# Kernel optimization log

Hardware: AMD Instinct MI355X
Metric: run time of the kernel (lower is better)

## Reference

```python
import jax, jax.numpy as jnp
import numpy as np

N, E, H, D, HC = 6000, 12000, 4, 32, 128


def _ln(x, g, b, eps=1e-5):
    m = jnp.mean(x, axis=-1, keepdims=True)
    v = jnp.mean((x - m) ** 2, axis=-1, keepdims=True)
    return (x - m) / jnp.sqrt(v + eps) * g + b


def _gelu(x):
    return jax.nn.gelu(x, approximate=False)


def _gatv2(x, src, dst, ea, wl, bl, wr, br, we, att, bias):
    # x: [N,HC], ea: [E,HC] (already encoded). heads H, per-head dim D.
    xl = (x @ wl + bl).reshape(N, H, D)   # source transform
    xr = (x @ wr + br).reshape(N, H, D)   # target transform
    xe = (ea @ we).reshape(E, H, D)
    g = jax.nn.leaky_relu(xl[src] + xr[dst] + xe, 0.1)   # [E,H,D]
    logits = jnp.einsum('ehd,hd->eh', g, att)            # [E,H]
    m = jax.ops.segment_max(logits, dst, num_segments=N)
    m = jnp.where(jnp.isfinite(m), m, 0.0)
    ex = jnp.exp(logits - m[dst])
    s = jax.ops.segment_sum(ex, dst, num_segments=N)
    alpha = ex / (s[dst] + 1e-16)                        # softmax over in-edges of dst
    out = jax.ops.segment_sum(alpha[..., None] * xl[src], dst, num_segments=N)
    return out.reshape(N, H * D) + bias


def _nnconv(h, src, dst, ea, w, b, root, bias):
    # dynamic per-edge weight matrix: [E, HC, HC]
    W = (ea @ w + b).reshape(E, HC, HC)
    msg = jnp.einsum('ei,eio->eo', h[src], W)            # per-edge matvec
    agg = jax.ops.segment_sum(msg, dst, num_segments=N)  # sum aggregation
    return agg + h @ root + bias


def setup_inputs() -> dict:
    key = jax.random.key(0)
    ks = jax.random.split(key, 16)
    rn = lambda k, shp, s: jax.random.normal(k, shp, jnp.float32) * s
    inv = lambda f: 1.0 / np.sqrt(f).astype(np.float32)
    return {
        'x': rn(ks[0], (N, 6), 1.0),
        'edge_index': jax.random.randint(ks[1], (2, E), 0, N, dtype=jnp.int32),
        'edge_attr': rn(ks[2], (E, 4), 1.0),
        'batch': jnp.zeros((N,), jnp.int32),
        'node_enc_w': rn(ks[3], (6, HC), inv(6)),
        'edge_enc_w': rn(ks[4], (4, HC), inv(4)),
        'edge_enc_b': jnp.zeros((HC,), jnp.float32),
        'gat_lin_l_w': rn(ks[5], (2, HC, HC), inv(HC)),
        'gat_lin_l_b': jnp.zeros((2, HC), jnp.float32),
        'gat_lin_r_w': rn(ks[6], (2, HC, HC), inv(HC)),
        'gat_lin_r_b': jnp.zeros((2, HC), jnp.float32),
        'gat_lin_e_w': rn(ks[7], (2, HC, HC), inv(HC)),
        'gat_att': rn(ks[8], (2, H, D), inv(D)),
        'gat_bias': jnp.zeros((2, HC), jnp.float32),
        'gat_ln_g': jnp.ones((2, HC), jnp.float32),
        'gat_ln_b': jnp.zeros((2, HC), jnp.float32),
        'nn_w': rn(ks[9], (8, HC, HC * HC), inv(HC)),
        'nn_b': jnp.zeros((8, HC * HC), jnp.float32),
        'nn_root': rn(ks[10], (8, HC, HC), inv(HC)),
        'nn_bias': jnp.zeros((8, HC), jnp.float32),
        'dec_ln_g': jnp.ones((8, HC), jnp.float32),
        'dec_ln_b': jnp.zeros((8, HC), jnp.float32),
        'out_w': rn(ks[11], (HC, 2), inv(HC)),
        'out_b': jnp.zeros((2,), jnp.float32),
    }


def reference(x, edge_index, edge_attr, batch, node_enc_w, edge_enc_w, edge_enc_b,
              gat_lin_l_w, gat_lin_l_b, gat_lin_r_w, gat_lin_r_b, gat_lin_e_w,
              gat_att, gat_bias, gat_ln_g, gat_ln_b,
              nn_w, nn_b, nn_root, nn_bias, dec_ln_g, dec_ln_b, out_w, out_b):
    src, dst = edge_index[0], edge_index[1]
    h0 = x @ node_enc_w                              # node encoder (no bias)
    ea = edge_attr @ edge_enc_w + edge_enc_b         # edge encoder
    # GraphTransEncoder layers (dropout in eval mode = identity)
    for i in range(2):
        x1 = _gatv2(h0, src, dst, ea, gat_lin_l_w[i], gat_lin_l_b[i],
                    gat_lin_r_w[i], gat_lin_r_b[i], gat_lin_e_w[i],
                    gat_att[i], gat_bias[i])
        h0 = _gelu(_ln(h0 + x1, gat_ln_g[i], gat_ln_b[i]))
    # initial conv with decoder[0]'s NNConv
    h = _nnconv(h0, src, dst, ea, nn_w[0], nn_b[0], nn_root[0], nn_bias[0])
    # DeepGCN 'res+' layers, each fed x + h
    for i in range(8):
        hin = h0 + h
        t = _gelu(_ln(hin, dec_ln_g[i], dec_ln_b[i]))
        t = _nnconv(t, src, dst, ea, nn_w[i], nn_b[i], nn_root[i], nn_bias[i])
        h = hin + t
    out = _gelu(_ln(h, dec_ln_g[0], dec_ln_b[0]))
    return out @ out_w + out_b
```

## Files before the change

### kernel.cpp

```cpp
#include <hip/hip_runtime.h>
#include <math.h>

#define NN 6000
#define NE 12000
#define DCAP 32

typedef _Float16 f16;
typedef _Float16 f16x8 __attribute__((ext_vector_type(8)));
typedef unsigned short u16x8 __attribute__((ext_vector_type(8)));
typedef float f32x4 __attribute__((ext_vector_type(4)));

__device__ __forceinline__ float gelu_f(float x) {
    return 0.5f * x * (1.0f + erff(x * 0.70710678118654752f));
}

__global__ __launch_bounds__(256) void k_pre_all(
    const float* __restrict__ nn_w, const float* __restrict__ nn_b,
    const float* __restrict__ nn_root, f16* __restrict__ bfh,
    const float* __restrict__ x, const float* __restrict__ node_w,
    float* __restrict__ h0, f16* __restrict__ hf,
    const int* __restrict__ ei, const float* __restrict__ eattr,
    int* __restrict__ cnt, float* __restrict__ ebs,
    const float* __restrict__ gat_e_w, const float* __restrict__ eew,
    const float* __restrict__ eeb, const float* __restrict__ lb,
    const float* __restrict__ rb, float* __restrict__ EW, float* __restrict__ biasLR,
    const float* __restrict__ gwl, const float* __restrict__ gwr,
    f16* __restrict__ WTh)
{
    __shared__ float enc[5][128];
    int b = blockIdx.x;
    int tid = threadIdx.x;
    if (b < 512) {
        for (int l = tid; l < 640; l += 256) {
            int j = l >> 7, k = l & 127;
            enc[j][k] = (j < 4) ? eew[j * 128 + k] : eeb[k];
        }
        __syncthreads();
        int gid = b * 256 + tid;
        int i = gid >> 14;
        int col = gid & 16383;
        int k_in = col >> 7, o = col & 127;
        const float* w = nn_w + (size_t)i * (128 * 16384) + col;
        float a0 = 0.f, a1 = 0.f, a2 = 0.f, a3 = 0.f, a4 = 0.f;
        #pragma unroll 8
        for (int k = 0; k < 128; ++k) {
            float wv = w[(size_t)k * 16384];
            a0 += enc[0][k] * wv; a1 += enc[1][k] * wv; a2 += enc[2][k] * wv;
            a3 += enc[3][k] * wv; a4 += enc[4][k] * wv;
        }
        a4 += nn_b[i * 16384 + col];
        float root = nn_root[(size_t)i * 16384 + col];
        float vals[6] = {a0, a1, a2, a3, a4, root};
        int ot = o >> 4, l15o = o & 15;
        size_t base_i = ((size_t)i * 8 + ot) * 24;
        #pragma unroll
        for (int j = 0; j < 6; ++j) {
            int c = j * 128 + k_in;
            int kb = c >> 5, lg = (c >> 3) & 3, jj = c & 7;
            size_t dst = ((base_i + kb) * 64 + lg * 16 + l15o) * 8 + jj;
            bfh[dst] = (f16)vals[j];
        }
    } else if (b < 3512) {
        int idx = (b - 512) * 256 + tid;
        int n = idx >> 7, c = idx & 127;
        float s = 0.f;
        #pragma unroll
        for (int f = 0; f < 6; ++f) s += x[n * 6 + f] * node_w[f * 128 + c];
        h0[idx] = s;
        hf[idx] = (f16)s;
    } else if (b < 3559) {
        int e = (b - 3512) * 256 + tid;
        if (e < NE) {
            int d = ei[NE + e];
            int pos = atomicAdd(&cnt[d], 1);
            if (pos < DCAP) {
                float* p = ebs + (size_t)(d * DCAP + pos) * 8;
                p[0] = __int_as_float(ei[e]);
                p[1] = eattr[e * 4 + 0];
                p[2] = eattr[e * 4 + 1];
                p[3] = eattr[e * 4 + 2];
                p[4] = eattr[e * 4 + 3];
            }
        }
    } else if (b < 3566) {
        int idx = (b - 3559) * 256 + tid;
        if (idx < 1280) {
            int i = idx / 640; int r = idx % 640; int j = r >> 7; int o = r & 127;
            float s = 0.f;
            for (int k = 0; k < 128; ++k) {
                float e = (j < 4) ? eew[j * 128 + k] : eeb[k];
                s += e * gat_e_w[i * 16384 + k * 128 + o];
            }
            EW[idx] = s;
        } else if (idx < 1792) {
            int j = idx - 1280; int i = j >> 8; int c = j & 255;
            biasLR[j] = (c < 128) ? lb[i * 128 + c] : rb[i * 128 + c - 128];
        }
    } else {
        int bb = b - 3566;
        int i = bb >> 2, half = (bb >> 1) & 1, piece = bb & 1;
        const float* s = (half ? gwr : gwl) + (size_t)i * 16384;
        size_t dbase = (size_t)i * 32768 + (size_t)half * 16384;
        for (int l = tid + piece * 8192; l < 8192 + piece * 8192; l += 256) {
            int o = l >> 7, k = l & 127;
            WTh[dbase + o * 128 + k] = (f16)s[k * 128 + o];
        }
    }
}

__global__ __launch_bounds__(256) void k_mm16(
    const f16* __restrict__ A, const f16* __restrict__ Bh,
    const float* __restrict__ bias, f16* __restrict__ C, int M, int P)
{
    __shared__ __align__(16) unsigned short smem[16384];
    unsigned short* sA  = smem;
    unsigned short* sBh = smem + 8192;
    const int tid = threadIdx.x;
    const int r0 = blockIdx.x * 64, n0 = blockIdx.y * 64;
    #pragma unroll
    for (int i = 0; i < 4; ++i) {
        int g = tid + i * 256; int row = g >> 4, u = g & 15;
        int dst = row * 128 + ((u ^ (row & 7)) << 3);
        int r = r0 + row;
        if (r < M) *(u16x8*)&sA[dst] = *(const u16x8*)((const unsigned short*)A + (size_t)r * 128 + u * 8);
        else { u16x8 z; for (int j = 0; j < 8; ++j) z[j] = 0; *(u16x8*)&sA[dst] = z; }
        size_t sb = (size_t)(n0 + row) * 128 + u * 8;
        *(u16x8*)&sBh[dst] = *(const u16x8*)((const unsigned short*)Bh + sb);
    }
    __syncthreads();
    const int lane = tid & 63, wid = tid >> 6;
    const int wm = wid & 1, wn = wid >> 1;
    const int l15 = lane & 15, lg = lane >> 4;
    f32x4 acc[2][2] = {};
    #pragma unroll
    for (int kk = 0; kk < 4; ++kk) {
        f16x8 a[2], bh_[2];
        #pragma unroll
        for (int fm = 0; fm < 2; ++fm) {
            int row = wm * 32 + fm * 16 + l15;
            int off = row * 128 + ((((kk << 2) + lg) ^ (row & 7)) << 3);
            a[fm] = *(const f16x8*)&sA[off];
        }
        #pragma unroll
        for (int fn = 0; fn < 2; ++fn) {
            int row = wn * 32 + fn * 16 + l15;
            int off = row * 128 + ((((kk << 2) + lg) ^ (row & 7)) << 3);
            bh_[fn] = *(const f16x8*)&sBh[off];
        }
        #pragma unroll
        for (int fm = 0; fm < 2; ++fm)
        #pragma unroll
        for (int fn = 0; fn < 2; ++fn)
            acc[fm][fn] = __builtin_amdgcn_mfma_f32_16x16x32_f16(a[fm], bh_[fn], acc[fm][fn], 0, 0, 0);
    }
    #pragma unroll
    for (int fn = 0; fn < 2; ++fn) {
        int col = n0 + wn * 32 + fn * 16 + l15;
        float bv = bias ? bias[col] : 0.f;
        #pragma unroll
        for (int fm = 0; fm < 2; ++fm) {
            int rbase = r0 + wm * 32 + fm * 16 + lg * 4;
            #pragma unroll
            for (int j = 0; j < 4; ++j) {
                int r = rbase + j;
                if (r < M) C[(size_t)r * P + col] = (f16)(acc[fm][fn][j] + bv);
            }
        }
    }
}

__global__ __launch_bounds__(256) void k_gat_fused(
    const f16* __restrict__ XLXR, const float* __restrict__ ebs,
    const int* __restrict__ cnt, const float* __restrict__ EW,
    const float* __restrict__ att, float* __restrict__ h0,
    const float* __restrict__ bias, const float* __restrict__ g,
    const float* __restrict__ b,
    f16* __restrict__ hf)
{
    __shared__ float slog[4][DCAP][4];
    __shared__ float sms[4][4][2];
    int rowl = threadIdx.x >> 6, lane = threadIdx.x & 63;
    int r = blockIdx.x * 4 + rowl;
    int deg = cnt[r]; if (deg > DCAP) deg = DCAP;
    int dc = (deg < 4) ? deg : 4;
    float hz0 = h0[r * 128 + lane], hz1 = h0[r * 128 + 64 + lane];
    float xr0 = (float)XLXR[r * 256 + 128 + lane];
    float xr1 = (float)XLXR[r * 256 + 192 + lane];
    float e0 = EW[lane], e1 = EW[128 + lane], e2 = EW[256 + lane], e3 = EW[384 + lane], e4 = EW[512 + lane];
    float f0 = EW[64 + lane], f1 = EW[192 + lane], f2 = EW[320 + lane], f3 = EW[448 + lane], f4 = EW[576 + lane];
    float at0 = att[lane], at1 = att[64 + lane];
    f32x4 q[4]; float a3v[4]; float xs0[4], xs1[4];
    #pragma unroll
    for (int j = 0; j < 4; ++j) {
        if (j < dc) {
            const float* ep = ebs + (size_t)(r * DCAP + j) * 8;
            q[j] = *(const f32x4*)ep;
            a3v[j] = ep[4];
        }
    }
    #pragma unroll
    for (int j = 0; j < 4; ++j) {
        if (j < dc) {
            int s = __float_as_int(q[j][0]);
            xs0[j] = (float)XLXR[s * 256 + lane];
            xs1[j] = (float)XLXR[s * 256 + 64 + lane];
        }
    }
    #pragma unroll
    for (int j = 0; j < 4; ++j) {
        if (j < dc) {
            float a0 = q[j][1], a1 = q[j][2], a2 = q[j][3], a3 = a3v[j];
            float g0 = xs0[j] + xr0 + (a0 * e0 + a1 * e1 + a2 * e2 + a3 * e3 + e4);
            float g1 = xs1[j] + xr1 + (a0 * f0 + a1 * f1 + a2 * f2 + a3 * f3 + f4);
            g0 = (g0 > 0.f) ? g0 : 0.1f * g0;
            g1 = (g1 > 0.f) ? g1 : 0.1f * g1;
            float p0 = g0 * at0, p1 = g1 * at1;
            for (int o = 16; o; o >>= 1) { p0 += __shfl_xor(p0, o, 32); p1 += __shfl_xor(p1, o, 32); }
            if ((lane & 31) == 0) {
                int hh2 = lane >> 5;
                slog[rowl][j][hh2] = p0;
                slog[rowl][j][2 + hh2] = p1;
            }
        }
    }
    for (int k = 4; k < deg; ++k) {
        const float* ep = ebs + (size_t)(r * DCAP + k) * 8;
        f32x4 qq = *(const f32x4*)ep;
        float a3 = ep[4];
        int s = __float_as_int(qq[0]);
        float a0 = qq[1], a1 = qq[2], a2 = qq[3];
        float g0 = (float)XLXR[s * 256 + lane]      + xr0 + (a0 * e0 + a1 * e1 + a2 * e2 + a3 * e3 + e4);
        float g1 = (float)XLXR[s * 256 + 64 + lane] + xr1 + (a0 * f0 + a1 * f1 + a2 * f2 + a3 * f3 + f4);
        g0 = (g0 > 0.f) ? g0 : 0.1f * g0;
        g1 = (g1 > 0.f) ? g1 : 0.1f * g1;
        float p0 = g0 * at0, p1 = g1 * at1;
        for (int o = 16; o; o >>= 1) { p0 += __shfl_xor(p0, o, 32); p1 += __shfl_xor(p1, o, 32); }
        if ((lane & 31) == 0) {
            int hh2 = lane >> 5;
            slog[rowl][k][hh2] = p0;
            slog[rowl][k][2 + hh2] = p1;
        }
    }
    if (lane < 4) {
        float mh = -1e30f;
        for (int k = 0; k < deg; ++k) mh = fmaxf(mh, slog[rowl][k][lane]);
        float sh = 0.f;
        for (int k = 0; k < deg; ++k) sh += expf(slog[rowl][k][lane] - mh);
        sms[rowl][lane][0] = mh; sms[rowl][lane][1] = sh;
    }
    int hd = lane >> 5;
    float m0 = sms[rowl][hd][0], s0 = sms[rowl][hd][1];
    float m1 = sms[rowl][2 + hd][0], s1 = sms[rowl][2 + hd][1];
    float acc0 = 0.f, acc1 = 0.f;
    #pragma unroll
    for (int j = 0; j < 4; ++j) {
        if (j < dc) {
            float al0 = expf(slog[rowl][j][hd] - m0) / (s0 + 1e-16f);
            float al1 = expf(slog[rowl][j][2 + hd] - m1) / (s1 + 1e-16f);
            acc0 += al0 * xs0[j];
            acc1 += al1 * xs1[j];
        }
    }
    for (int k = 4; k < deg; ++k) {
        int s = __float_as_int(ebs[(size_t)(r * DCAP + k) * 8]);
        float al0 = expf(slog[rowl][k][hd] - m0) / (s0 + 1e-16f);
        float al1 = expf(slog[rowl][k][2 + hd] - m1) / (s1 + 1e-16f);
        acc0 += al0 * (float)XLXR[s * 256 + lane];
        acc1 += al1 * (float)XLXR[s * 256 + 64 + lane];
    }
    float v0 = hz0 + acc0 + bias[lane];
    float v1 = hz1 + acc1 + bias[64 + lane];
    float sum = v0 + v1;
    for (int o = 32; o; o >>= 1) sum += __shfl_xor(sum, o, 64);
    float mean = sum * 0.0078125f;
    float d0 = v0 - mean, d1 = v1 - mean;
    float var = d0 * d0 + d1 * d1;
    for (int o = 32; o; o >>= 1) var += __shfl_xor(var, o, 64);
    float inv = rsqrtf(var * 0.0078125f + 1e-5f);
    float y0 = gelu_f(d0 * inv * g[lane] + b[lane]);
    float y1 = gelu_f(d1 * inv * g[64 + lane] + b[64 + lane]);
    h0[r * 128 + lane] = y0; h0[r * 128 + 64 + lane] = y1;
    hf[r * 128 + lane] = (f16)y0;
    hf[r * 128 + 64 + lane] = (f16)y1;
}

__global__ __launch_bounds__(512) void k_conv(
    const float* __restrict__ ebs, const int* __restrict__ cnt,
    const f16* __restrict__ TF,
    const f16* __restrict__ BFh,
    const float* __restrict__ bias,
    const float* __restrict__ h0, float* __restrict__ HIN,
    const float* __restrict__ lng, const float* __restrict__ lnb,
    f16* __restrict__ TFout, int kind,
    const float* __restrict__ outw, const float* __restrict__ outb,
    float* __restrict__ outp)
{
    __shared__ __align__(16) unsigned short sA[16 * 768];
    const int tid = threadIdx.x;
    const int r0 = blockIdx.x * 8;
    const int lane = tid & 63, w = tid >> 6;
    const int l15 = lane & 15, lg = lane >> 4;

    {
        unsigned int* zp = (unsigned int*)&sA[(8 + w) * 768];
        #pragma unroll
        for (int z = 0; z < 6; ++z) zp[lane + z * 64] = 0;
    }

    int r = r0 + w;
    int deg = cnt[r]; if (deg > DCAP) deg = DCAP;
    float bs0 = bias[lane], bs1 = bias[64 + lane];
    float lg0 = lng[lane], lg1 = lng[64 + lane];
    float lb0 = lnb[lane], lb1 = lnb[64 + lane];
    float h00 = 0.f, h01 = 0.f, hi0 = 0.f, hi1 = 0.f;
    if (kind != 2) {
        h00 = h0[r * 128 + lane];
        h01 = h0[r * 128 + 64 + lane];
    }
    if (kind != 0) {
        hi0 = HIN[r * 128 + lane];
        hi1 = HIN[r * 128 + 64 + lane];
    }
    unsigned int rtv = *(const unsigned int*)&TF[(size_t)r * 128 + lane * 2];
    float acc[5][2] = {};
    for (int k0 = 0; k0 < deg; k0 += 4) {
        int km = deg - k0; if (km > 4) km = 4;
        f32x4 q[4]; float a3v[4]; unsigned int tt[4];
        #pragma unroll
        for (int j = 0; j < 4; ++j) {
            if (j < km) {
                const float* ep = ebs + (size_t)(r * DCAP + k0 + j) * 8;
                q[j] = *(const f32x4*)ep;
                a3v[j] = ep[4];
            }
        }
        #pragma unroll
        for (int j = 0; j < 4; ++j) {
            if (j < km) {
                int s = __float_as_int(q[j][0]);
                tt[j] = *(const unsigned int*)&TF[(size_t)s * 128 + lane * 2];
            }
        }
        #pragma unroll
        for (int j = 0; j < 4; ++j) {
            if (j < km) {
                float a0 = q[j][1], a1 = q[j][2], a2 = q[j][3], a3 = a3v[j];
                float t0 = (float)__builtin_bit_cast(f16, (unsigned short)(tt[j] & 0xffff));
                float t1 = (float)__builtin_bit_cast(f16, (unsigned short)(tt[j] >> 16));
                acc[0][0] += a0 * t0; acc[1][0] += a1 * t0; acc[2][0] += a2 * t0;
                acc[3][0] += a3 * t0; acc[4][0] += t0;
                acc[0][1] += a0 * t1; acc[1][1] += a1 * t1; acc[2][1] += a2 * t1;
                acc[3][1] += a3 * t1; acc[4][1] += t1;
            }
        }
    }
    {
        int row = w;
        int rw = row & 7;
        #pragma unroll
        for (int j = 0; j < 5; ++j) {
            int u = j * 16 + (lane >> 2);
            int us = (u & ~7) | ((u & 7) ^ rw);
            unsigned short p0 = __builtin_bit_cast(unsigned short, (f16)acc[j][0]);
            unsigned short p1 = __builtin_bit_cast(unsigned short, (f16)acc[j][1]);
            *(unsigned int*)&sA[row * 768 + us * 8 + ((2 * lane) & 7)] =
                (unsigned int)p0 | ((unsigned int)p1 << 16);
        }
        int u = 80 + (lane >> 2);
        int us = (u & ~7) | ((u & 7) ^ rw);
        *(unsigned int*)&sA[row * 768 + us * 8 + ((2 * lane) & 7)] = rtv;
    }
    __syncthreads();

    f32x4 acc2 = {};
    const f16* bhp = BFh + ((size_t)w * 24) * 512 + (size_t)lane * 8;
    #pragma unroll
    for (int kb = 0; kb < 24; ++kb) {
        f16x8 bhv = *(const f16x8*)(bhp + (size_t)kb * 512);
        int row = l15;
        int u = kb * 4 + lg;
        int us = (u & ~7) | ((u & 7) ^ (row & 7));
        f16x8 a = *(const f16x8*)&sA[row * 768 + us * 8];
        acc2 = __builtin_amdgcn_mfma_f32_16x16x32_f16(a, bhv, acc2, 0, 0, 0);
    }
    __syncthreads();
    float* sOut = (float*)sA;
    {
        int col = w * 16 + l15;
        #pragma unroll
        for (int j = 0; j < 4; ++j) {
            int row = lg * 4 + j;
            if (row < 8) sOut[row * 132 + col] = acc2[j];
        }
    }
    __syncthreads();

    {
        float c0 = bs0 + sOut[w * 132 + lane];
        float c1 = bs1 + sOut[w * 132 + 64 + lane];
        float u0, u1;
        if (kind == 0) {
            u0 = h00 + c0;
            u1 = h01 + c1;
            HIN[r * 128 + lane] = u0; HIN[r * 128 + 64 + lane] = u1;
        } else if (kind == 1) {
            u0 = hi0 + h00 + c0;
            u1 = hi1 + h01 + c1;
            HIN[r * 128 + lane] = u0; HIN[r * 128 + 64 + lane] = u1;
        } else {
            u0 = hi0 + c0;
            u1 = hi1 + c1;
        }
        float sum = u0 + u1;
        for (int o = 32; o; o >>= 1) sum += __shfl_xor(sum, o, 64);
        float mean = sum * 0.0078125f;
        float d0 = u0 - mean, d1 = u1 - mean;
        float var = d0 * d0 + d1 * d1;
        for (int o = 32; o; o >>= 1) var += __shfl_xor(var, o, 64);
        float inv = rsqrtf(var * 0.0078125f + 1e-5f);
        float y0 = gelu_f(d0 * inv * lg0 + lb0);
        float y1 = gelu_f(d1 * inv * lg1 + lb1);
        if (kind != 2) {
            TFout[r * 128 + lane] = (f16)y0;
            TFout[r * 128 + 64 + lane] = (f16)y1;
        } else {
            float p0 = y0 * outw[lane * 2 + 0] + y1 * outw[(64 + lane) * 2 + 0];
            float p1 = y0 * outw[lane * 2 + 1] + y1 * outw[(64 + lane) * 2 + 1];
            for (int o = 32; o; o >>= 1) { p0 += __shfl_xor(p0, o, 64); p1 += __shfl_xor(p1, o, 64); }
            if (lane == 0) {
                outp[r * 2 + 0] = p0 + outb[0];
                outp[r * 2 + 1] = p1 + outb[1];
            }
        }
    }
}

extern "C" void kernel_launch(void* const* d_in, const int* in_sizes, int n_in,
                              void* d_out, int out_size, void* d_ws, size_t ws_size,
                              hipStream_t stream)
{
    const float* x        = (const float*)d_in[0];
    const int*   ei       = (const int*)d_in[1];
    const float* eattr    = (const float*)d_in[2];
    const float* node_w   = (const float*)d_in[4];
    const float* eew      = (const float*)d_in[5];
    const float* eeb      = (const float*)d_in[6];
    const float* gat_l_w  = (const float*)d_in[7];
    const float* gat_l_b  = (const float*)d_in[8];
    const float* gat_r_w  = (const float*)d_in[9];
    const float* gat_r_b  = (const float*)d_in[10];
    const float* gat_e_w  = (const float*)d_in[11];
    const float* gat_att  = (const float*)d_in[12];
    const float* gat_bias = (const float*)d_in[13];
    const float* gat_ln_g = (const float*)d_in[14];
    const float* gat_ln_b = (const float*)d_in[15];
    const float* nn_w     = (const float*)d_in[16];
    const float* nn_b     = (const float*)d_in[17];
    const float* nn_root  = (const float*)d_in[18];
    const float* nn_bias  = (const float*)d_in[19];
    const float* dec_g    = (const float*)d_in[20];
    const float* dec_b    = (const float*)d_in[21];
    const float* out_w    = (const float*)d_in[22];
    const float* out_b    = (const float*)d_in[23];
    float* out = (float*)d_out;

    float* ws    = (float*)d_ws;
    float* EW    = ws;
    float* BLR   = EW + 1280;
    float* H0    = BLR + 512;
    float* HIN   = H0 + 768000;
    int*   CNT   = (int*)(HIN + 768000);
    float* EBS   = (float*)(CNT + 6000);
    f16*   BFh   = (f16*)(EBS + 1536000);
    f16*   WTh   = BFh + 786432;
    f16*   H0F   = WTh + 65536;
    f16*   TF0   = H0F + 768000;
    f16*   TF1   = TF0 + 768000;
    f16*   XLXRh = TF1 + 768000;

    dim3 b256(256), b512(512);
    hipMemsetAsync(CNT, 0, NN * sizeof(int), stream);
    hipLaunchKernelGGL(k_pre_all, dim3(3574), b256, 0, stream,
                       nn_w, nn_b, nn_root, BFh,
                       x, node_w, H0, H0F, ei, eattr, CNT, EBS,
                       gat_e_w, eew, eeb, gat_l_b, gat_r_b, EW, BLR,
                       gat_l_w, gat_r_w, WTh);

    for (int i = 0; i < 2; ++i) {
        hipLaunchKernelGGL(k_mm16, dim3(94, 4), b256, 0, stream,
                           H0F, WTh + i * 32768,
                           BLR + i * 256, XLXRh, NN, 256);
        hipLaunchKernelGGL(k_gat_fused, dim3(1500), b256, 0, stream,
                           XLXRh, EBS, CNT, EW + i * 640, gat_att + i * 128,
                           H0, gat_bias + i * 128, gat_ln_g + i * 128, gat_ln_b + i * 128,
                           (i == 0) ? H0F : TF0);
    }

    hipLaunchKernelGGL(k_conv, dim3(750), b512, 0, stream,
                       EBS, CNT, TF0, BFh, nn_bias,
                       H0, HIN, dec_g, dec_b, TF1, 0,
                       (const float*)nullptr, (const float*)nullptr, (float*)nullptr);

    for (int i = 0; i < 8; ++i) {
        int fin = (i == 7);
        const f16* tin  = (i & 1) ? TF0 : TF1;
        f16*       tout = (i & 1) ? TF1 : TF0;
        hipLaunchKernelGGL(k_conv, dim3(750), b512, 0, stream,
                           EBS, CNT, tin,
                           BFh + (size_t)i * 98304,
                           nn_bias + i * 128, H0, HIN,
                           fin ? dec_g : dec_g + (i + 1) * 128,
                           fin ? dec_b : dec_b + (i + 1) * 128,
                           tout, fin ? 2 : 1, out_w, out_b, out);
    }
}
```

Before: 161.9 us.

## Shrink NNConv blocks to four rows with two MFMA column tiles per wave

The NNConv kernel now runs 256-thread blocks that each handle 4 destination rows instead of 8. Each wave computes two 16-column output tiles, so each A fragment loaded from LDS feeds two MFMAs, and the zero-padded LDS rows are no longer needed. The grid doubles to 1500 blocks to improve occupancy and load balance. In exchange, only 4 of the 16 MFMA rows carry useful data, so matrix-core utilization drops and each block loads B weights for fewer rows.

Result: slower. 200.1 us (+23.6%).

```diff
diff --git a/kernel.cpp b/kernel.cpp
--- a/kernel.cpp
+++ b/kernel.cpp
@@ -284,7 +284,7 @@
     hf[r * 128 + 64 + lane] = (f16)y1;
 }
 
-__global__ __launch_bounds__(512) void k_conv(
+__global__ __launch_bounds__(256) void k_conv(
     const float* __restrict__ ebs, const int* __restrict__ cnt,
     const f16* __restrict__ TF,
     const f16* __restrict__ BFh,
@@ -295,17 +295,11 @@
     const float* __restrict__ outw, const float* __restrict__ outb,
     float* __restrict__ outp)
 {
-    __shared__ __align__(16) unsigned short sA[16 * 768];
+    __shared__ __align__(16) unsigned short sA[4 * 768];
     const int tid = threadIdx.x;
-    const int r0 = blockIdx.x * 8;
+    const int r0 = blockIdx.x * 4;
     const int lane = tid & 63, w = tid >> 6;
     const int l15 = lane & 15, lg = lane >> 4;
-
-    {
-        unsigned int* zp = (unsigned int*)&sA[(8 + w) * 768];
-        #pragma unroll
-        for (int z = 0; z < 6; ++z) zp[lane + z * 64] = 0;
-    }
 
     int r = r0 + w;
     int deg = cnt[r]; if (deg > DCAP) deg = DCAP;
@@ -356,41 +350,44 @@
     }
     {
         int row = w;
-        int rw = row & 7;
         #pragma unroll
         for (int j = 0; j < 5; ++j) {
             int u = j * 16 + (lane >> 2);
-            int us = (u & ~7) | ((u & 7) ^ rw);
+            int us = (u & ~7) | ((u & 7) ^ row);
             unsigned short p0 = __builtin_bit_cast(unsigned short, (f16)acc[j][0]);
             unsigned short p1 = __builtin_bit_cast(unsigned short, (f16)acc[j][1]);
             *(unsigned int*)&sA[row * 768 + us * 8 + ((2 * lane) & 7)] =
                 (unsigned int)p0 | ((unsigned int)p1 << 16);
         }
         int u = 80 + (lane >> 2);
-        int us = (u & ~7) | ((u & 7) ^ rw);
+        int us = (u & ~7) | ((u & 7) ^ row);
         *(unsigned int*)&sA[row * 768 + us * 8 + ((2 * lane) & 7)] = rtv;
     }
     __syncthreads();
 
-    f32x4 acc2 = {};
-    const f16* bhp = BFh + ((size_t)w * 24) * 512 + (size_t)lane * 8;
+    f32x4 acc2[2] = {};
+    const f16* bhp0 = BFh + ((size_t)(2 * w) * 24) * 512 + (size_t)lane * 8;
+    const f16* bhp1 = bhp0 + (size_t)24 * 512;
     #pragma unroll
     for (int kb = 0; kb < 24; ++kb) {
-        f16x8 bhv = *(const f16x8*)(bhp + (size_t)kb * 512);
-        int row = l15;
+        int row = l15 & 3;
         int u = kb * 4 + lg;
-        int us = (u & ~7) | ((u & 7) ^ (row & 7));
+        int us = (u & ~7) | ((u & 7) ^ row);
         f16x8 a = *(const f16x8*)&sA[row * 768 + us * 8];
-        acc2 = __builtin_amdgcn_mfma_f32_16x16x32_f16(a, bhv, acc2, 0, 0, 0);
+        f16x8 b0 = *(const f16x8*)(bhp0 + (size_t)kb * 512);
+        f16x8 b1 = *(const f16x8*)(bhp1 + (size_t)kb * 512);
+        acc2[0] = __builtin_amdgcn_mfma_f32_16x16x32_f16(a, b0, acc2[0], 0, 0, 0);
+        acc2[1] = __builtin_amdgcn_mfma_f32_16x16x32_f16(a, b1, acc2[1], 0, 0, 0);
     }
     __syncthreads();
     float* sOut = (float*)sA;
-    {
-        int col = w * 16 + l15;
-        #pragma unroll
-        for (int j = 0; j < 4; ++j) {
-            int row = lg * 4 + j;
-            if (row < 8) sOut[row * 132 + col] = acc2[j];
+    #pragma unroll
+    for (int t = 0; t < 2; ++t) {
+        int col = (2 * w + t) * 16 + l15;
+        if (lg == 0) {
+            #pragma unroll
+            for (int j = 0; j < 4; ++j)
+                sOut[j * 132 + col] = acc2[t][j];
         }
     }
     __syncthreads();
@@ -478,7 +475,7 @@
     f16*   TF1   = TF0 + 768000;
     f16*   XLXRh = TF1 + 768000;
 
-    dim3 b256(256), b512(512);
+    dim3 b256(256);
     hipMemsetAsync(CNT, 0, NN * sizeof(int), stream);
     hipLaunchKernelGGL(k_pre_all, dim3(3574), b256, 0, stream,
                        nn_w, nn_b, nn_root, BFh,
@@ -496,7 +493,7 @@
                            (i == 0) ? H0F : TF0);
     }
 
-    hipLaunchKernelGGL(k_conv, dim3(750), b512, 0, stream,
+    hipLaunchKernelGGL(k_conv, dim3(1500), b256, 0, stream,
                        EBS, CNT, TF0, BFh, nn_bias,
                        H0, HIN, dec_g, dec_b, TF1, 0,
                        (const float*)nullptr, (const float*)nullptr, (float*)nullptr);
@@ -505,7 +502,7 @@
         int fin = (i == 7);
         const f16* tin  = (i & 1) ? TF0 : TF1;
         f16*       tout = (i & 1) ? TF1 : TF0;
-        hipLaunchKernelGGL(k_conv, dim3(750), b512, 0, stream,
+        hipLaunchKernelGGL(k_conv, dim3(1500), b256, 0, stream,
                            EBS, CNT, tin,
                            BFh + (size_t)i * 98304,
                            nn_bias + i * 128, H0, HIN,
```
